# Kernel tuning notes

Measured on AMD Instinct MI355X. Metric: run time of the kernel, lower is better.

## Reference

```python
import jax, jax.numpy as jnp
import numpy as np

B, H, W = 16, 1024, 1024
EPS = 1e-7
FG_PROB = 0.1  # foreground pixel probability for synthetic gt


def setup_inputs() -> dict:
    key = jax.random.key(0)
    k1, k2 = jax.random.split(key)
    probs = jax.random.normal(k1, (B, 2, H, W), dtype=jnp.float32)
    gt = (jax.random.uniform(k2, (B, H, W)) < FG_PROB).astype(jnp.float32)
    gt_f_num = gt.sum(axis=(1, 2))  # per-sample foreground pixel count (float)
    return {"probs": probs, "gt": gt, "gt_f_num": gt_f_num, "img_h": H, "img_w": W}


def reference(probs, gt, gt_f_num, img_h, img_w):
    # foreground probability, clamped
    pc = jax.nn.softmax(probs, axis=1)[:, 1, :, :]
    pc = jnp.clip(pc, EPS, 1.0 - EPS)
    b = pc.shape[0]
    f_loss = -(gt * jnp.log(pc)).reshape(b, -1)          # [B, N]
    b_loss = -((1.0 - gt) * jnp.log(1.0 - pc)).reshape(b, -1)  # [B, N]
    n = b_loss.shape[1]

    # sort background loss descending per sample; top gt_f_num[i] entries are
    # "difficult" negatives, the rest are "simple" (equivalent to the torch
    # gather-into-zero-buffers since only sums/counts are taken afterwards)
    sorted_b = -jnp.sort(-b_loss, axis=1)                # descending, [B, N]
    k = gt_f_num.astype(jnp.int32)                       # int(gt_f_num[i])
    mask = jnp.arange(n, dtype=jnp.int32)[None, :] < k[:, None]  # [B, N]

    difficult_sum = jnp.sum(jnp.where(mask, sorted_b, 0.0), axis=1)
    simple_sum = jnp.sum(jnp.where(mask, 0.0, sorted_b), axis=1)
    difficult_num = jnp.sum(mask & (sorted_b != 0.0), axis=1).astype(jnp.float32)

    difficult_b_loss = difficult_sum / (difficult_num + 1e-16)
    simple_b_loss = simple_sum / (float(img_h * img_w) + 1e-16)
    f_loss_mean = f_loss.sum(axis=1) / (gt_f_num + 1e-16)

    return difficult_b_loss.mean() + f_loss_mean.mean() + simple_b_loss.mean()
```

## Files before the change

### kernel.cpp

```cpp
#include <hip/hip_runtime.h>
#include <math.h>

#define NB 16
#define NPIX 1048576
#define BINS 4096
#define HBINS (BINS / 2)
#define DUMMY_W HBINS
#define CHUNKS 64
#define TPB_A 256
#define PIX_PER_BLOCK (NPIX / CHUNKS)
#define PPT 4
#define ITERS_A (PIX_PER_BLOCK / (TPB_A * PPT))
#define TPB_B 256
#define BINS_PER_CHUNK (BINS / TPB_B)
#define WORDS_PER_THREAD (HBINS / TPB_B)
#define BLOSS_MAX 16.2f
#define BINW (BLOSS_MAX / (float)BINS)
#define B_CAP 15.9424f
#define F_CAP 16.1181f

typedef float f32x4 __attribute__((ext_vector_type(4)));

__global__ __launch_bounds__(TPB_A, 8) void pass_a(
    const float* __restrict__ probs, const float* __restrict__ gt,
    unsigned* __restrict__ g_hist, float* __restrict__ f_part,
    float* __restrict__ b_part)
{
    __shared__ unsigned s_cnt[HBINS + 8];
    __shared__ float s_redf[TPB_A / 64];
    __shared__ float s_redb[TPB_A / 64];

    const int tid = threadIdx.x;
    for (int j = tid; j < HBINS + 8; j += TPB_A) s_cnt[j] = 0u;
    __syncthreads();

    const int blk = blockIdx.x;
    const int b = blk / CHUNKS;
    const int chunk = blk % CHUNKS;
    const float* p0 = probs + (size_t)b * 2 * NPIX;
    const float* p1 = p0 + NPIX;
    const float* gp = gt + (size_t)b * NPIX;
    const int base = chunk * PIX_PER_BLOCK;
    const float scale = (float)BINS / BLOSS_MAX;

    float f_acc = 0.f, b_acc = 0.f;

    for (int it = 0; it < ITERS_A; ++it) {
        const int i = base + it * (TPB_A * PPT) + (tid << 2);
        const f32x4 a = *(const f32x4*)(p0 + i);
        const f32x4 c = *(const f32x4*)(p1 + i);
        const f32x4 g = *(const f32x4*)(gp + i);
        const float dv[PPT] = {c.x - a.x, c.y - a.y, c.z - a.z, c.w - a.w};
        const float gv[PPT] = {g.x, g.y, g.z, g.w};
        #pragma unroll
        for (int q = 0; q < PPT; ++q) {
            const float d = dv[q];
            const float sp = fmaxf(d, 0.f) + __logf(1.f + __expf(-fabsf(d)));
            const bool fg = gv[q] > 0.5f;
            const float fl = fminf(sp - d, F_CAP);
            const float bl = fminf(sp, B_CAP);
            f_acc += fg ? fl : 0.f;
            b_acc += fg ? 0.f : bl;
            int bin = (int)(bl * scale);
            bin = bin < (BINS - 1) ? bin : (BINS - 1);
            const int word = fg ? DUMMY_W : (bin >> 1);
            const unsigned inc = 1u << ((bin & 1) << 4);
            atomicAdd(&s_cnt[word], inc);
        }
    }
    __syncthreads();

    unsigned* dst = g_hist + ((size_t)b * CHUNKS + chunk) * HBINS;
    for (int j = tid; j < HBINS; j += TPB_A) dst[j] = s_cnt[j];

    #pragma unroll
    for (int o = 32; o > 0; o >>= 1) {
        f_acc += __shfl_down(f_acc, o, 64);
        b_acc += __shfl_down(b_acc, o, 64);
    }
    if ((tid & 63) == 0) { s_redf[tid >> 6] = f_acc; s_redb[tid >> 6] = b_acc; }
    __syncthreads();
    if (tid == 0) {
        float f = 0.f, bs = 0.f;
        #pragma unroll
        for (int w = 0; w < TPB_A / 64; ++w) { f += s_redf[w]; bs += s_redb[w]; }
        f_part[b * CHUNKS + chunk] = f;
        b_part[b * CHUNKS + chunk] = bs;
    }
}

__global__ __launch_bounds__(TPB_B) void pass_b(
    const unsigned* __restrict__ g_hist, const float* __restrict__ f_part,
    const float* __restrict__ b_part, const float* __restrict__ gt_f_num,
    float* __restrict__ terms)
{
    __shared__ unsigned s_suf[TPB_B];
    __shared__ double s_wsuf[TPB_B];
    __shared__ double s_dsum;
    __shared__ double s_fb[2];

    const int b = blockIdx.x;
    const int t = threadIdx.x;

    unsigned cnt[BINS_PER_CHUNK];
    #pragma unroll
    for (int j = 0; j < BINS_PER_CHUNK; ++j) cnt[j] = 0u;
    const unsigned* hb = g_hist + (size_t)b * CHUNKS * HBINS + t * WORDS_PER_THREAD;
    #pragma unroll 4
    for (int c = 0; c < CHUNKS; ++c) {
        const uint4 w0 = *(const uint4*)(hb + (size_t)c * HBINS);
        const uint4 w1 = *(const uint4*)(hb + (size_t)c * HBINS + 4);
        cnt[0]  += w0.x & 0xFFFFu;  cnt[1]  += w0.x >> 16;
        cnt[2]  += w0.y & 0xFFFFu;  cnt[3]  += w0.y >> 16;
        cnt[4]  += w0.z & 0xFFFFu;  cnt[5]  += w0.z >> 16;
        cnt[6]  += w0.w & 0xFFFFu;  cnt[7]  += w0.w >> 16;
        cnt[8]  += w1.x & 0xFFFFu;  cnt[9]  += w1.x >> 16;
        cnt[10] += w1.y & 0xFFFFu;  cnt[11] += w1.y >> 16;
        cnt[12] += w1.z & 0xFFFFu;  cnt[13] += w1.z >> 16;
        cnt[14] += w1.w & 0xFFFFu;  cnt[15] += w1.w >> 16;
    }

    const int cb = t * BINS_PER_CHUNK;
    unsigned c = 0; double w = 0.0;
    #pragma unroll
    for (int j = 0; j < BINS_PER_CHUNK; ++j) {
        c += cnt[j];
        w += (double)cnt[j] * (double)(((float)(cb + j) + 0.5f) * BINW);
    }
    s_suf[t] = c; s_wsuf[t] = w;

    if (t < 64) {
        double ff = (double)f_part[b * CHUNKS + t];
        double bb = (double)b_part[b * CHUNKS + t];
        #pragma unroll
        for (int o = 32; o > 0; o >>= 1) {
            ff += __shfl_down(ff, o, 64);
            bb += __shfl_down(bb, o, 64);
        }
        if (t == 0) { s_fb[0] = ff; s_fb[1] = bb; }
    }
    __syncthreads();

    for (int off = 1; off < TPB_B; off <<= 1) {
        const unsigned ac = (t + off < TPB_B) ? s_suf[t + off] : 0u;
        const double aw = (t + off < TPB_B) ? s_wsuf[t + off] : 0.0;
        __syncthreads();
        s_suf[t] += ac; s_wsuf[t] += aw;
        __syncthreads();
    }

    const long long kk = (long long)gt_f_num[b];
    const unsigned long long n_pos = (unsigned long long)s_suf[0];
    const unsigned long long suf_me = s_suf[t];
    const unsigned long long suf_nx = (t + 1 < TPB_B) ? s_suf[t + 1] : 0ull;

    if (kk > 0 && (unsigned long long)kk < n_pos &&
        suf_nx < (unsigned long long)kk && (unsigned long long)kk <= suf_me) {
        unsigned long long cum = suf_nx;
        double W = (t + 1 < TPB_B) ? s_wsuf[t + 1] : 0.0;
        int bstar = cb;
        for (int j = BINS_PER_CHUNK - 1; j >= 0; --j) {
            const unsigned cc = cnt[j];
            if (cum + cc >= (unsigned long long)kk) { bstar = cb + j; break; }
            cum += cc;
            W += (double)cc * (double)(((float)(cb + j) + 0.5f) * BINW);
        }
        const double partial = (double)(kk - (long long)cum);
        s_dsum = W + partial * (double)(((float)bstar + 0.5f) * BINW);
    }
    __syncthreads();

    if (t == 0) {
        const double S_total = s_fb[1];
        const double fs = s_fb[0];
        const double gfn = (double)gt_f_num[b];
        double dsum, dnum;
        if (kk <= 0) { dsum = 0.0; dnum = 0.0; }
        else if ((unsigned long long)kk >= n_pos) { dsum = S_total; dnum = (double)n_pos; }
        else { dsum = s_dsum; dnum = (double)kk; }
        const double term = dsum / (dnum + 1e-16)
                          + fs / (gfn + 1e-16)
                          + (S_total - dsum) / ((double)NPIX + 1e-16);
        terms[b] = (float)term;
    }
}

__global__ void pass_c(const float* __restrict__ terms, float* __restrict__ out)
{
    if (threadIdx.x == 0 && blockIdx.x == 0) {
        float s = 0.f;
        #pragma unroll
        for (int i = 0; i < NB; ++i) s += terms[i];
        out[0] = s / (float)NB;
    }
}

extern "C" void kernel_launch(void* const* d_in, const int* in_sizes, int n_in,
                              void* d_out, int out_size, void* d_ws, size_t ws_size,
                              hipStream_t stream) {
    const float* probs = (const float*)d_in[0];
    const float* gt    = (const float*)d_in[1];
    const float* gfn   = (const float*)d_in[2];
    char* ws = (char*)d_ws;

    const size_t hist_bytes = (size_t)NB * CHUNKS * HBINS * sizeof(unsigned);
    unsigned* g_hist = (unsigned*)ws;
    float*    f_part = (float*)(ws + hist_bytes);
    float*    b_part = f_part + NB * CHUNKS;
    float*    terms  = b_part + NB * CHUNKS;

    hipLaunchKernelGGL(pass_a, dim3(NB * CHUNKS), dim3(TPB_A), 0, stream,
                       probs, gt, g_hist, f_part, b_part);
    hipLaunchKernelGGL(pass_b, dim3(NB), dim3(TPB_B), 0, stream,
                       g_hist, f_part, b_part, gfn, terms);
    hipLaunchKernelGGL(pass_c, dim3(1), dim3(64), 0, stream,
                       terms, (float*)d_out);
}
```

Before: 253.2 us.

## Pack count and fixed-point loss sum into 64-bit histogram bins with privatized copies

Replaces the 4096-bin packed 16-bit count histogram with 2048 bins of 64-bit words that hold both a count (upper bits) and a fixed-point sum of the background loss (lower 44 bits). Each bin is duplicated across two copies keyed by thread parity to reduce LDS atomic contention, and the block size doubles to 512 threads. The partial-bin contribution now uses the bin's actual mean loss instead of the bin centre, which should improve accuracy with fewer bins. In exchange it costs 64-bit LDS atomics, a larger shared footprint (32 KB) that may limit occupancy, and twice the global histogram traffic per bin.

After: 282.6 us. 1.12x slower.

```diff
diff --git a/kernel.cpp b/kernel.cpp
--- a/kernel.cpp
+++ b/kernel.cpp
@@ -3,35 +3,36 @@
 
 #define NB 16
 #define NPIX 1048576
-#define BINS 4096
-#define HBINS (BINS / 2)
-#define DUMMY_W HBINS
+#define BINS 2048
+#define COPIES 2
 #define CHUNKS 64
-#define TPB_A 256
+#define TPB_A 512
 #define PIX_PER_BLOCK (NPIX / CHUNKS)
 #define PPT 4
 #define ITERS_A (PIX_PER_BLOCK / (TPB_A * PPT))
 #define TPB_B 256
-#define BINS_PER_CHUNK (BINS / TPB_B)
-#define WORDS_PER_THREAD (HBINS / TPB_B)
+#define BINS_PER_T (BINS / TPB_B)
 #define BLOSS_MAX 16.2f
 #define BINW (BLOSS_MAX / (float)BINS)
 #define B_CAP 15.9424f
 #define F_CAP 16.1181f
+#define FIX_SCALE 16777216.0f
+#define INV_FIX (1.0 / 16777216.0)
+#define SUM_MASK ((1ull << 44) - 1)
 
 typedef float f32x4 __attribute__((ext_vector_type(4)));
 
 __global__ __launch_bounds__(TPB_A, 8) void pass_a(
     const float* __restrict__ probs, const float* __restrict__ gt,
-    unsigned* __restrict__ g_hist, float* __restrict__ f_part,
+    unsigned long long* __restrict__ g_hist, float* __restrict__ f_part,
     float* __restrict__ b_part)
 {
-    __shared__ unsigned s_cnt[HBINS + 8];
+    __shared__ unsigned long long s_hist[BINS * COPIES];
     __shared__ float s_redf[TPB_A / 64];
     __shared__ float s_redb[TPB_A / 64];
 
     const int tid = threadIdx.x;
-    for (int j = tid; j < HBINS + 8; j += TPB_A) s_cnt[j] = 0u;
+    for (int j = tid; j < BINS * COPIES; j += TPB_A) s_hist[j] = 0ull;
     __syncthreads();
 
     const int blk = blockIdx.x;
@@ -42,6 +43,7 @@
     const float* gp = gt + (size_t)b * NPIX;
     const int base = chunk * PIX_PER_BLOCK;
     const float scale = (float)BINS / BLOSS_MAX;
+    const int copy = tid & 1;
 
     float f_acc = 0.f, b_acc = 0.f;
 
@@ -63,15 +65,16 @@
             b_acc += fg ? 0.f : bl;
             int bin = (int)(bl * scale);
             bin = bin < (BINS - 1) ? bin : (BINS - 1);
-            const int word = fg ? DUMMY_W : (bin >> 1);
-            const unsigned inc = 1u << ((bin & 1) << 4);
-            atomicAdd(&s_cnt[word], inc);
-        }
-    }
-    __syncthreads();
-
-    unsigned* dst = g_hist + ((size_t)b * CHUNKS + chunk) * HBINS;
-    for (int j = tid; j < HBINS; j += TPB_A) dst[j] = s_cnt[j];
+            const unsigned long long inc = fg ? 0ull
+                : ((1ull << 44) | (unsigned long long)(unsigned)(bl * FIX_SCALE));
+            atomicAdd(&s_hist[(bin << 1) | copy], inc);
+        }
+    }
+    __syncthreads();
+
+    unsigned long long* dst = g_hist + ((size_t)b * CHUNKS + chunk) * BINS;
+    for (int j = tid; j < BINS; j += TPB_A)
+        dst[j] = s_hist[2 * j] + s_hist[2 * j + 1];
 
     #pragma unroll
     for (int o = 32; o > 0; o >>= 1) {
@@ -90,7 +93,7 @@
 }
 
 __global__ __launch_bounds__(TPB_B) void pass_b(
-    const unsigned* __restrict__ g_hist, const float* __restrict__ f_part,
+    const unsigned long long* __restrict__ g_hist, const float* __restrict__ f_part,
     const float* __restrict__ b_part, const float* __restrict__ gt_f_num,
     float* __restrict__ terms)
 {
@@ -102,30 +105,25 @@
     const int b = blockIdx.x;
     const int t = threadIdx.x;
 
-    unsigned cnt[BINS_PER_CHUNK];
+    unsigned cnt[BINS_PER_T];
+    unsigned long long smf[BINS_PER_T];
     #pragma unroll
-    for (int j = 0; j < BINS_PER_CHUNK; ++j) cnt[j] = 0u;
-    const unsigned* hb = g_hist + (size_t)b * CHUNKS * HBINS + t * WORDS_PER_THREAD;
-    #pragma unroll 4
+    for (int j = 0; j < BINS_PER_T; ++j) { cnt[j] = 0u; smf[j] = 0ull; }
+    const unsigned long long* hb = g_hist + (size_t)b * CHUNKS * BINS + t * BINS_PER_T;
     for (int c = 0; c < CHUNKS; ++c) {
-        const uint4 w0 = *(const uint4*)(hb + (size_t)c * HBINS);
-        const uint4 w1 = *(const uint4*)(hb + (size_t)c * HBINS + 4);
-        cnt[0]  += w0.x & 0xFFFFu;  cnt[1]  += w0.x >> 16;
-        cnt[2]  += w0.y & 0xFFFFu;  cnt[3]  += w0.y >> 16;
-        cnt[4]  += w0.z & 0xFFFFu;  cnt[5]  += w0.z >> 16;
-        cnt[6]  += w0.w & 0xFFFFu;  cnt[7]  += w0.w >> 16;
-        cnt[8]  += w1.x & 0xFFFFu;  cnt[9]  += w1.x >> 16;
-        cnt[10] += w1.y & 0xFFFFu;  cnt[11] += w1.y >> 16;
-        cnt[12] += w1.z & 0xFFFFu;  cnt[13] += w1.z >> 16;
-        cnt[14] += w1.w & 0xFFFFu;  cnt[15] += w1.w >> 16;
-    }
-
-    const int cb = t * BINS_PER_CHUNK;
+        #pragma unroll
+        for (int j = 0; j < BINS_PER_T; ++j) {
+            const unsigned long long v = hb[(size_t)c * BINS + j];
+            cnt[j] += (unsigned)(v >> 44);
+            smf[j] += (v & SUM_MASK);
+        }
+    }
+
     unsigned c = 0; double w = 0.0;
     #pragma unroll
-    for (int j = 0; j < BINS_PER_CHUNK; ++j) {
+    for (int j = 0; j < BINS_PER_T; ++j) {
         c += cnt[j];
-        w += (double)cnt[j] * (double)(((float)(cb + j) + 0.5f) * BINW);
+        w += (double)smf[j] * INV_FIX;
     }
     s_suf[t] = c; s_wsuf[t] = w;
 
@@ -158,15 +156,18 @@
         suf_nx < (unsigned long long)kk && (unsigned long long)kk <= suf_me) {
         unsigned long long cum = suf_nx;
         double W = (t + 1 < TPB_B) ? s_wsuf[t + 1] : 0.0;
-        int bstar = cb;
-        for (int j = BINS_PER_CHUNK - 1; j >= 0; --j) {
+        double part = 0.0;
+        for (int j = BINS_PER_T - 1; j >= 0; --j) {
             const unsigned cc = cnt[j];
-            if (cum + cc >= (unsigned long long)kk) { bstar = cb + j; break; }
+            const double sv = (double)smf[j] * INV_FIX;
+            if (cum + cc >= (unsigned long long)kk) {
+                part = (double)(kk - (long long)cum) * (sv / (double)cc);
+                break;
+            }
             cum += cc;
-            W += (double)cc * (double)(((float)(cb + j) + 0.5f) * BINW);
-        }
-        const double partial = (double)(kk - (long long)cum);
-        s_dsum = W + partial * (double)(((float)bstar + 0.5f) * BINW);
+            W += sv;
+        }
+        s_dsum = W + part;
     }
     __syncthreads();
 
@@ -203,11 +204,11 @@
     const float* gfn   = (const float*)d_in[2];
     char* ws = (char*)d_ws;
 
-    const size_t hist_bytes = (size_t)NB * CHUNKS * HBINS * sizeof(unsigned);
-    unsigned* g_hist = (unsigned*)ws;
-    float*    f_part = (float*)(ws + hist_bytes);
-    float*    b_part = f_part + NB * CHUNKS;
-    float*    terms  = b_part + NB * CHUNKS;
+    const size_t hist_bytes = (size_t)NB * CHUNKS * BINS * sizeof(unsigned long long);
+    unsigned long long* g_hist = (unsigned long long*)ws;
+    float* f_part = (float*)(ws + hist_bytes);
+    float* b_part = f_part + NB * CHUNKS;
+    float* terms  = b_part + NB * CHUNKS;
 
     hipLaunchKernelGGL(pass_a, dim3(NB * CHUNKS), dim3(TPB_A), 0, stream,
                        probs, gt, g_hist, f_part, b_part);
```
